# Performance work log

Measured on AMD Instinct MI355X. Metric: run time of the kernel, lower is better.

## Reference

```python
import jax, jax.numpy as jnp
import numpy as np

N_NODES = 100000


def _graph_conv(x, src, dst, d_out_isqrt, d_in_isqrt, W, b):
    # DGL GraphConv, norm='both': scale by D_out^{-1/2} at src, sum to dst,
    # scale by D_in^{-1/2}, then dense transform + bias.
    h = x * d_out_isqrt[:, None]
    agg = jax.ops.segment_sum(h[src], dst, num_segments=N_NODES)  # [N, d]
    agg = agg * d_in_isqrt[:, None]
    return agg @ W + b


def setup_inputs() -> dict:
    key = jax.random.key(0)
    ks = jax.random.split(key, 10)
    E = 1600000
    return {
        "feat": jax.random.normal(ks[0], (N_NODES, 64), jnp.float32),
        "src": jax.random.randint(ks[1], (E,), 0, N_NODES, dtype=jnp.int32),
        "dst": jax.random.randint(ks[2], (E,), 0, N_NODES, dtype=jnp.int32),
        "eps": jax.random.normal(ks[3], (N_NODES, 32), jnp.float32),
        "W1": jax.random.normal(ks[4], (64, 64), jnp.float32) * 0.1,
        "b1": jnp.zeros((64,), jnp.float32),
        "W2": jax.random.normal(ks[5], (64, 64), jnp.float32) * 0.1,
        "b2": jnp.zeros((64,), jnp.float32),
        "Wm": jax.random.normal(ks[6], (64, 32), jnp.float32) * 0.1,
        "bm": jnp.zeros((32,), jnp.float32),
    }


def reference(feat, src, dst, eps, W1, b1, W2, b2, Wm, bm):
    ones = jnp.ones(src.shape, feat.dtype)
    d_out = jax.ops.segment_sum(ones, src, num_segments=N_NODES)
    d_in = jax.ops.segment_sum(ones, dst, num_segments=N_NODES)
    d_out_isqrt = jax.lax.rsqrt(jnp.maximum(d_out, 1.0))
    d_in_isqrt = jax.lax.rsqrt(jnp.maximum(d_in, 1.0))

    h = jnp.tanh(_graph_conv(feat, src, dst, d_out_isqrt, d_in_isqrt, W1, b1))
    h = jax.nn.relu(_graph_conv(h, src, dst, d_out_isqrt, d_in_isqrt, W2, b2))
    # NOTE: source code uses dec_mean for BOTH mean and log_std (dec_log_std unused).
    z_mean = _graph_conv(h, src, dst, d_out_isqrt, d_in_isqrt, Wm, bm)
    z_log_std = _graph_conv(h, src, dst, d_out_isqrt, d_in_isqrt, Wm, bm)
    z_adj = z_mean + jnp.exp(z_log_std) * eps  # reparameterized torch.normal
    return (z_adj, z_log_std, z_mean)
```

## Files before the change

### kernel.cpp

```cpp
#include <hip/hip_runtime.h>
#include <math.h>

#define N_NODES 100000
#define NBUK 256
#define BNODES ((N_NODES + NBUK - 1) / NBUK)
#define BCAP 10240
#define CHUNK 16384

__device__ __forceinline__ unsigned bf16rne(float f) {
    unsigned u = __float_as_uint(f);
    return (u + 0x7FFFu + ((u >> 16) & 1u)) >> 16;
}

__global__ __launch_bounds__(256) void pass1_kernel(const int* __restrict__ src,
                                                    const int* __restrict__ dst,
                                                    int* __restrict__ bcnt_d,
                                                    int* __restrict__ bcnt_s,
                                                    unsigned int* __restrict__ dstream,
                                                    unsigned short* __restrict__ sstream, int E) {
    __shared__ int hd[NBUK];
    __shared__ int hs[NBUK];
    const int t = threadIdx.x;
    const int cbase = blockIdx.x * CHUNK;
    const int csize = min(CHUNK, E - cbase);

    hd[t] = 0;
    hs[t] = 0;
    __syncthreads();
    for (int i = t; i < csize; i += 256) {
        int d = dst[cbase + i];
        int s = src[cbase + i];
        atomicAdd(&hd[d / BNODES], 1);
        atomicAdd(&hs[s / BNODES], 1);
    }
    __syncthreads();
    int myd = atomicAdd(&bcnt_d[t], hd[t]);
    int mys = atomicAdd(&bcnt_s[t], hs[t]);
    hd[t] = myd;
    hs[t] = mys;
    __syncthreads();
    for (int i = t; i < csize; i += 256) {
        int d = dst[cbase + i];
        int s = src[cbase + i];
        int bd = d / BNODES;
        int bs = s / BNODES;
        int slot = atomicAdd(&hd[bd], 1);
        if (slot < BCAP)
            dstream[(size_t)bd * BCAP + slot] = ((unsigned)s << 9) | (unsigned)(d - bd * BNODES);
        int slot2 = atomicAdd(&hs[bs], 1);
        if (slot2 < BCAP)
            sstream[(size_t)bs * BCAP + slot2] = (unsigned short)(s - bs * BNODES);
    }
}

__global__ void bucket_base_kernel(const int* __restrict__ bcnt_d, int* __restrict__ csr_base,
                                   int* __restrict__ row_start) {
    __shared__ int lds[NBUK];
    int t = threadIdx.x;
    int v = min(bcnt_d[t], BCAP);
    lds[t] = v;
    __syncthreads();
    for (int off = 1; off < NBUK; off <<= 1) {
        int y = (t >= off) ? lds[t - off] : 0;
        __syncthreads();
        lds[t] += y;
        __syncthreads();
    }
    csr_base[t] = lds[t] - v;
    if (t == NBUK - 1) row_start[N_NODES] = lds[NBUK - 1];
}

__global__ __launch_bounds__(256) void pass2_dst_kernel(const unsigned int* __restrict__ dstream,
                                                        const int* __restrict__ bcnt_d,
                                                        const int* __restrict__ csr_base,
                                                        float* __restrict__ isi,
                                                        int* __restrict__ row_start,
                                                        int* __restrict__ csr_src) {
    __shared__ int cnt[512];
    __shared__ int pfx[512];
    __shared__ int wsum[256];
    const int b = blockIdx.x;
    const int t = threadIdx.x;
    const int m = min(bcnt_d[b], BCAP);
    const int base = csr_base[b];
    const int nbeg = b * BNODES;
    const int nn = min(BNODES, N_NODES - nbeg);
    const unsigned int* eb = dstream + (size_t)b * BCAP;

    cnt[t] = 0;
    cnt[t + 256] = 0;
    __syncthreads();
    for (int i = t; i < m; i += 256) atomicAdd(&cnt[eb[i] & 511], 1);
    __syncthreads();
    int c0 = cnt[2 * t], c1 = cnt[2 * t + 1];
    int s = c0 + c1;
    wsum[t] = s;
    __syncthreads();
    for (int off = 1; off < 256; off <<= 1) {
        int y = (t >= off) ? wsum[t - off] : 0;
        __syncthreads();
        wsum[t] += y;
        __syncthreads();
    }
    int excl = wsum[t] - s;
    pfx[2 * t] = excl;
    pfx[2 * t + 1] = excl + c0;
    __syncthreads();
    for (int j = t; j < nn; j += 256) {
        isi[nbeg + j] = rsqrtf(fmaxf((float)cnt[j], 1.0f));
        row_start[nbeg + j] = base + pfx[j];
    }
    __syncthreads();
    cnt[t] = pfx[t];
    cnt[t + 256] = pfx[t + 256];
    __syncthreads();
    for (int i = t; i < m; i += 256) {
        unsigned int p = eb[i];
        int dl = p & 511;
        int sv = p >> 9;
        int pos = atomicAdd(&cnt[dl], 1);
        csr_src[base + pos] = sv;
    }
}

__global__ __launch_bounds__(256) void pass2_src_kernel(const unsigned short* __restrict__ sstream,
                                                        const int* __restrict__ bcnt_s,
                                                        float* __restrict__ iso) {
    __shared__ int cnt[512];
    const int b = blockIdx.x;
    const int t = threadIdx.x;
    const int m = min(bcnt_s[b], BCAP);
    const int nbeg = b * BNODES;
    const int nn = min(BNODES, N_NODES - nbeg);
    const unsigned short* eb = sstream + (size_t)b * BCAP;

    cnt[t] = 0;
    cnt[t + 256] = 0;
    __syncthreads();
    for (int i = t; i < m; i += 256) atomicAdd(&cnt[eb[i]], 1);
    __syncthreads();
    for (int j = t; j < nn; j += 256) iso[nbeg + j] = rsqrtf(fmaxf((float)cnt[j], 1.0f));
}

template <int DOUT, bool BF16OUT>
__global__ __launch_bounds__(256) void gemm_scale_kernel(const float* __restrict__ x,
                                                         const float* __restrict__ W,
                                                         const float* __restrict__ iso,
                                                         void* __restrict__ out_, int n) {
    constexpr int TC = DOUT / 4;
    constexpr int TR = 256 / TC;
    constexpr int ROWS = TR * 4;

    __shared__ float Xs[64 * ROWS];
    __shared__ float Ws[64 * DOUT];

    const int t = threadIdx.x;
    const int row_base = blockIdx.x * ROWS;

    {
        const float4* Wg = reinterpret_cast<const float4*>(W);
        float4* Ws4 = reinterpret_cast<float4*>(Ws);
        for (int i = t; i < 64 * TC; i += 256) Ws4[i] = Wg[i];
    }
    {
        const float4* xg = reinterpret_cast<const float4*>(x);
#pragma unroll
        for (int it = 0; it < ROWS / 16; ++it) {
            int f = t + it * 256;
            int r = f >> 4;
            int kq = f & 15;
            int row = row_base + r;
            int rcl = row < n ? row : n - 1;
            float4 v = xg[(size_t)rcl * 16 + kq];
            int rp = r ^ ((kq & 7) << 2);
            Xs[(kq * 4 + 0) * ROWS + rp] = v.x;
            Xs[(kq * 4 + 1) * ROWS + rp] = v.y;
            Xs[(kq * 4 + 2) * ROWS + rp] = v.z;
            Xs[(kq * 4 + 3) * ROWS + rp] = v.w;
        }
    }
    __syncthreads();

    const int tc = t % TC;
    const int tr = t / TC;

    float acc[4][4];
#pragma unroll
    for (int i = 0; i < 4; ++i)
#pragma unroll
        for (int j = 0; j < 4; ++j) acc[i][j] = 0.0f;

    const float4* Xs4 = reinterpret_cast<const float4*>(Xs);
    const float4* Ws4 = reinterpret_cast<const float4*>(Ws);

#pragma unroll 8
    for (int k = 0; k < 64; ++k) {
        float4 a = Xs4[k * (ROWS / 4) + (tr ^ ((k >> 2) & 7))];
        float4 b = Ws4[k * TC + tc];
        acc[0][0] += a.x * b.x; acc[0][1] += a.x * b.y; acc[0][2] += a.x * b.z; acc[0][3] += a.x * b.w;
        acc[1][0] += a.y * b.x; acc[1][1] += a.y * b.y; acc[1][2] += a.y * b.z; acc[1][3] += a.y * b.w;
        acc[2][0] += a.z * b.x; acc[2][1] += a.z * b.y; acc[2][2] += a.z * b.z; acc[2][3] += a.z * b.w;
        acc[3][0] += a.w * b.x; acc[3][1] += a.w * b.y; acc[3][2] += a.w * b.z; acc[3][3] += a.w * b.w;
    }

#pragma unroll
    for (int i = 0; i < 4; ++i) {
        int row = row_base + tr * 4 + i;
        if (row < n) {
            float sc = iso[row];
            if (BF16OUT) {
                unsigned b0 = bf16rne(acc[i][0] * sc);
                unsigned b1 = bf16rne(acc[i][1] * sc);
                unsigned b2 = bf16rne(acc[i][2] * sc);
                unsigned b3 = bf16rne(acc[i][3] * sc);
                uint2 o;
                o.x = (b1 << 16) | b0;
                o.y = (b3 << 16) | b2;
                reinterpret_cast<uint2*>(out_)[(size_t)row * TC + tc] = o;
            } else {
                float4 o;
                o.x = acc[i][0] * sc;
                o.y = acc[i][1] * sc;
                o.z = acc[i][2] * sc;
                o.w = acc[i][3] * sc;
                reinterpret_cast<float4*>(out_)[(size_t)row * TC + tc] = o;
            }
        }
    }
}

template <int MODE>
__global__ __launch_bounds__(256) void gather64_bf16_kernel(const unsigned int* __restrict__ h2,
                                                            const int* __restrict__ csr_src,
                                                            const int* __restrict__ row_start,
                                                            const float* __restrict__ isi,
                                                            const float* __restrict__ b,
                                                            float* __restrict__ out, int n) {
    int g = threadIdx.x >> 5;
    int j = threadIdx.x & 31;
    int node = blockIdx.x * 8 + g;
    if (node >= n) return;

    int beg = row_start[node];
    int end = row_start[node + 1];
    float acc0 = 0.0f, acc1 = 0.0f;
    int e = beg;
    for (; e + 4 <= end; e += 4) {
        int s0 = csr_src[e + 0];
        int s1 = csr_src[e + 1];
        int s2 = csr_src[e + 2];
        int s3 = csr_src[e + 3];
        unsigned p0 = h2[(size_t)s0 * 32 + j];
        unsigned p1 = h2[(size_t)s1 * 32 + j];
        unsigned p2 = h2[(size_t)s2 * 32 + j];
        unsigned p3 = h2[(size_t)s3 * 32 + j];
        acc0 += __uint_as_float(p0 << 16) + __uint_as_float(p1 << 16) +
                __uint_as_float(p2 << 16) + __uint_as_float(p3 << 16);
        acc1 += __uint_as_float(p0 & 0xFFFF0000u) + __uint_as_float(p1 & 0xFFFF0000u) +
                __uint_as_float(p2 & 0xFFFF0000u) + __uint_as_float(p3 & 0xFFFF0000u);
    }
    for (; e < end; ++e) {
        unsigned p = h2[(size_t)csr_src[e] * 32 + j];
        acc0 += __uint_as_float(p << 16);
        acc1 += __uint_as_float(p & 0xFFFF0000u);
    }

    float sc = isi[node];
    float v0 = acc0 * sc + b[2 * j];
    float v1 = acc1 * sc + b[2 * j + 1];
    if (MODE == 0) {
        v0 = tanhf(v0);
        v1 = tanhf(v1);
    } else {
        v0 = fmaxf(v0, 0.0f);
        v1 = fmaxf(v1, 0.0f);
    }
    float2 o = make_float2(v0, v1);
    reinterpret_cast<float2*>(out)[(size_t)node * 32 + j] = o;
}

__global__ void gather32_final_kernel(const float* __restrict__ h, const int* __restrict__ csr_src,
                                      const int* __restrict__ row_start, const float* __restrict__ isi,
                                      const float* __restrict__ b, const float* __restrict__ eps,
                                      float* __restrict__ out, int n) {
    const int D = 32;
    int g = threadIdx.x / D;
    int j = threadIdx.x % D;
    int node = blockIdx.x * 8 + g;
    if (node >= n) return;

    int beg = row_start[node];
    int end = row_start[node + 1];
    float acc = 0.0f;
    int e = beg;
    for (; e + 4 <= end; e += 4) {
        int s0 = csr_src[e + 0];
        int s1 = csr_src[e + 1];
        int s2 = csr_src[e + 2];
        int s3 = csr_src[e + 3];
        acc += h[(long long)s0 * D + j] + h[(long long)s1 * D + j] +
               h[(long long)s2 * D + j] + h[(long long)s3 * D + j];
    }
    for (; e < end; ++e) acc += h[(long long)csr_src[e] * D + j];

    float v = acc * isi[node] + b[j];
    const int total = N_NODES * 32;
    int i = node * 32 + j;
    out[i] = v + expf(v) * eps[i];
    out[total + i] = v;
    out[2 * total + i] = v;
}

static inline size_t align_up(size_t x, size_t a) { return (x + a - 1) & ~(a - 1); }

extern "C" void kernel_launch(void* const* d_in, const int* in_sizes, int n_in,
                              void* d_out, int out_size, void* d_ws, size_t ws_size,
                              hipStream_t stream) {
    const float* feat = (const float*)d_in[0];
    const int* src = (const int*)d_in[1];
    const int* dst = (const int*)d_in[2];
    const float* eps = (const float*)d_in[3];
    const float* W1 = (const float*)d_in[4];
    const float* b1 = (const float*)d_in[5];
    const float* W2 = (const float*)d_in[6];
    const float* b2 = (const float*)d_in[7];
    const float* Wm = (const float*)d_in[8];
    const float* bm = (const float*)d_in[9];

    const int N = N_NODES;
    const int E = in_sizes[1];
    float* out = (float*)d_out;

    char* ws = (char*)d_ws;
    size_t off = 0;
    float* iso     = (float*)(ws + off); off = align_up(off + (size_t)N * 4, 256);
    float* isi     = (float*)(ws + off); off = align_up(off + (size_t)N * 4, 256);
    int* row_start = (int*)(ws + off); off = align_up(off + (size_t)(N + 1) * 4, 256);
    int* csr_base  = (int*)(ws + off); off = align_up(off + (size_t)NBUK * 4, 256);
    int* bcnt_d    = (int*)(ws + off); off = align_up(off + (size_t)NBUK * 4, 256);
    int* bcnt_s    = (int*)(ws + off); off = align_up(off + (size_t)NBUK * 4, 256);
    int* csr_src   = (int*)(ws + off); off = align_up(off + (size_t)E * 4, 256);
    float* bufA    = (float*)(ws + off); off = align_up(off + (size_t)N * 64 * 4, 256);
    float* bufH    = (float*)(ws + off); off = align_up(off + (size_t)N * 64 * 4, 256);
    (void)ws_size;
    unsigned int* dstream = (unsigned int*)bufA;
    unsigned short* sstream = (unsigned short*)((char*)bufA + (size_t)NBUK * BCAP * 4);
    unsigned int* bufA_bf16 = (unsigned int*)bufA;

    const int B = 256;
    const int nchunks = (E + CHUNK - 1) / CHUNK;

    hipMemsetAsync(bcnt_d, 0, (size_t)NBUK * 4, stream);
    hipMemsetAsync(bcnt_s, 0, (size_t)NBUK * 4, stream);
    pass1_kernel<<<nchunks, B, 0, stream>>>(src, dst, bcnt_d, bcnt_s, dstream, sstream, E);
    bucket_base_kernel<<<1, NBUK, 0, stream>>>(bcnt_d, csr_base, row_start);
    pass2_dst_kernel<<<NBUK, B, 0, stream>>>(dstream, bcnt_d, csr_base, isi, row_start, csr_src);
    pass2_src_kernel<<<NBUK, B, 0, stream>>>(sstream, bcnt_s, iso);

    gemm_scale_kernel<64, true><<<(N + 63) / 64, B, 0, stream>>>(feat, W1, iso, bufA_bf16, N);
    gather64_bf16_kernel<0><<<(N + 7) / 8, B, 0, stream>>>(bufA_bf16, csr_src, row_start, isi, b1, bufH, N);

    gemm_scale_kernel<64, true><<<(N + 63) / 64, B, 0, stream>>>(bufH, W2, iso, bufA_bf16, N);
    gather64_bf16_kernel<1><<<(N + 7) / 8, B, 0, stream>>>(bufA_bf16, csr_src, row_start, isi, b2, bufH, N);

    gemm_scale_kernel<32, false><<<(N + 127) / 128, B, 0, stream>>>(bufH, Wm, iso, bufA, N);
    gather32_final_kernel<<<(N + 7) / 8, B, 0, stream>>>(bufA, csr_src, row_start, isi, bm, eps, out, N);
}
```

Before: 373.5 us.

## Split edge bucketing into histogram, scan and scatter passes with smaller chunks

The single bucketing pass, which both histogrammed and scattered edges using global atomics on the per-bucket counters, is replaced by a three-stage multisplit. First a per-chunk histogram kernel runs, then a two-level scan over chunk groups, then a scatter kernel that uses the precomputed offsets. The chunk size drops from 16384 to 2048 so many more blocks run in parallel, and the edge ordering within each bucket becomes deterministic. In exchange the edge arrays are read twice, and three extra small launches are added, two of them with very little parallelism.

```diff
diff --git a/kernel.cpp b/kernel.cpp
--- a/kernel.cpp
+++ b/kernel.cpp
@@ -5,25 +5,23 @@
 #define NBUK 256
 #define BNODES ((N_NODES + NBUK - 1) / NBUK)
 #define BCAP 10240
-#define CHUNK 16384
+#define CHUNK 2048
+#define NGRP 8
 
 __device__ __forceinline__ unsigned bf16rne(float f) {
     unsigned u = __float_as_uint(f);
     return (u + 0x7FFFu + ((u >> 16) & 1u)) >> 16;
 }
 
-__global__ __launch_bounds__(256) void pass1_kernel(const int* __restrict__ src,
+__global__ __launch_bounds__(256) void hist1_kernel(const int* __restrict__ src,
                                                     const int* __restrict__ dst,
-                                                    int* __restrict__ bcnt_d,
-                                                    int* __restrict__ bcnt_s,
-                                                    unsigned int* __restrict__ dstream,
-                                                    unsigned short* __restrict__ sstream, int E) {
+                                                    int* __restrict__ hist_d,
+                                                    int* __restrict__ hist_s, int E) {
     __shared__ int hd[NBUK];
     __shared__ int hs[NBUK];
     const int t = threadIdx.x;
     const int cbase = blockIdx.x * CHUNK;
     const int csize = min(CHUNK, E - cbase);
-
     hd[t] = 0;
     hs[t] = 0;
     __syncthreads();
@@ -34,23 +32,42 @@
         atomicAdd(&hs[s / BNODES], 1);
     }
     __syncthreads();
-    int myd = atomicAdd(&bcnt_d[t], hd[t]);
-    int mys = atomicAdd(&bcnt_s[t], hs[t]);
-    hd[t] = myd;
-    hs[t] = mys;
-    __syncthreads();
-    for (int i = t; i < csize; i += 256) {
-        int d = dst[cbase + i];
-        int s = src[cbase + i];
-        int bd = d / BNODES;
-        int bs = s / BNODES;
-        int slot = atomicAdd(&hd[bd], 1);
-        if (slot < BCAP)
-            dstream[(size_t)bd * BCAP + slot] = ((unsigned)s << 9) | (unsigned)(d - bd * BNODES);
-        int slot2 = atomicAdd(&hs[bs], 1);
-        if (slot2 < BCAP)
-            sstream[(size_t)bs * BCAP + slot2] = (unsigned short)(s - bs * BNODES);
-    }
+    hist_d[(size_t)blockIdx.x * NBUK + t] = hd[t];
+    hist_s[(size_t)blockIdx.x * NBUK + t] = hs[t];
+}
+
+__global__ void local_scan_kernel(int* __restrict__ hist_d, int* __restrict__ hist_s,
+                                  int* __restrict__ part_d, int* __restrict__ part_s,
+                                  int nch, int cpg) {
+    const int t = threadIdx.x;
+    const int side = blockIdx.x & 1;
+    const int g = blockIdx.x >> 1;
+    int* hist = side ? hist_s : hist_d;
+    int* part = side ? part_s : part_d;
+    int c0 = g * cpg;
+    int c1 = min(nch, c0 + cpg);
+    int run = 0;
+    for (int c = c0; c < c1; ++c) {
+        int v = hist[(size_t)c * NBUK + t];
+        hist[(size_t)c * NBUK + t] = run;
+        run += v;
+    }
+    part[g * NBUK + t] = run;
+}
+
+__global__ void group_scan_kernel(int* __restrict__ part_d, int* __restrict__ part_s,
+                                  int* __restrict__ bcnt_d, int* __restrict__ bcnt_s) {
+    const int t = threadIdx.x;
+    int* part = blockIdx.x ? part_s : part_d;
+    int* bcnt = blockIdx.x ? bcnt_s : bcnt_d;
+    int run = 0;
+#pragma unroll
+    for (int g = 0; g < NGRP; ++g) {
+        int v = part[g * NBUK + t];
+        part[g * NBUK + t] = run;
+        run += v;
+    }
+    bcnt[t] = run;
 }
 
 __global__ void bucket_base_kernel(const int* __restrict__ bcnt_d, int* __restrict__ csr_base,
@@ -68,6 +85,39 @@
     }
     csr_base[t] = lds[t] - v;
     if (t == NBUK - 1) row_start[N_NODES] = lds[NBUK - 1];
+}
+
+__global__ __launch_bounds__(256) void scatter_ms_kernel(const int* __restrict__ src,
+                                                         const int* __restrict__ dst,
+                                                         const int* __restrict__ hist_d,
+                                                         const int* __restrict__ hist_s,
+                                                         const int* __restrict__ part_d,
+                                                         const int* __restrict__ part_s,
+                                                         unsigned int* __restrict__ dstream,
+                                                         unsigned short* __restrict__ sstream,
+                                                         int E, int cpg) {
+    __shared__ int cd[NBUK];
+    __shared__ int cs[NBUK];
+    const int t = threadIdx.x;
+    const int c = blockIdx.x;
+    const int g = c / cpg;
+    const int cbase = c * CHUNK;
+    const int csize = min(CHUNK, E - cbase);
+    cd[t] = hist_d[(size_t)c * NBUK + t] + part_d[g * NBUK + t];
+    cs[t] = hist_s[(size_t)c * NBUK + t] + part_s[g * NBUK + t];
+    __syncthreads();
+    for (int i = t; i < csize; i += 256) {
+        int d = dst[cbase + i];
+        int s = src[cbase + i];
+        int bd = d / BNODES;
+        int bs = s / BNODES;
+        int slot = atomicAdd(&cd[bd], 1);
+        if (slot < BCAP)
+            dstream[(size_t)bd * BCAP + slot] = ((unsigned)s << 9) | (unsigned)(d - bd * BNODES);
+        int slot2 = atomicAdd(&cs[bs], 1);
+        if (slot2 < BCAP)
+            sstream[(size_t)bs * BCAP + slot2] = (unsigned short)(s - bs * BNODES);
+    }
 }
 
 __global__ __launch_bounds__(256) void pass2_dst_kernel(const unsigned int* __restrict__ dstream,
@@ -346,14 +396,21 @@
     unsigned int* dstream = (unsigned int*)bufA;
     unsigned short* sstream = (unsigned short*)((char*)bufA + (size_t)NBUK * BCAP * 4);
     unsigned int* bufA_bf16 = (unsigned int*)bufA;
+    const int nch = (E + CHUNK - 1) / CHUNK;
+    const int cpg = (nch + NGRP - 1) / NGRP;
+    int* hist_d = (int*)bufH;
+    int* hist_s = hist_d + (size_t)nch * NBUK;
+    int* part_d = hist_s + (size_t)nch * NBUK;
+    int* part_s = part_d + (size_t)NGRP * NBUK;
 
     const int B = 256;
-    const int nchunks = (E + CHUNK - 1) / CHUNK;
-
-    hipMemsetAsync(bcnt_d, 0, (size_t)NBUK * 4, stream);
-    hipMemsetAsync(bcnt_s, 0, (size_t)NBUK * 4, stream);
-    pass1_kernel<<<nchunks, B, 0, stream>>>(src, dst, bcnt_d, bcnt_s, dstream, sstream, E);
+
+    hist1_kernel<<<nch, B, 0, stream>>>(src, dst, hist_d, hist_s, E);
+    local_scan_kernel<<<2 * NGRP, B, 0, stream>>>(hist_d, hist_s, part_d, part_s, nch, cpg);
+    group_scan_kernel<<<2, B, 0, stream>>>(part_d, part_s, bcnt_d, bcnt_s);
     bucket_base_kernel<<<1, NBUK, 0, stream>>>(bcnt_d, csr_base, row_start);
+    scatter_ms_kernel<<<nch, B, 0, stream>>>(src, dst, hist_d, hist_s, part_d, part_s,
+                                             dstream, sstream, E, cpg);
     pass2_dst_kernel<<<NBUK, B, 0, stream>>>(dstream, bcnt_d, csr_base, isi, row_start, csr_src);
     pass2_src_kernel<<<NBUK, B, 0, stream>>>(sstream, bcnt_s, iso);
 
```

Result: no change. 378.5 us (+1.3%).
